# Kernel tuning notes

Measured on AMD Instinct MI355X. Metric: run time of the kernel, lower is better.

The kernel has to match this reference:

```python
import jax, jax.numpy as jnp
import numpy as np

K = 2  # diffusion order
N, S, D, L, C = 4000, 32, 128, 2, 10
THETA = 0.5


def setup_inputs() -> dict:
    key = jax.random.key(0)
    ks = jax.random.split(key, 16)
    w = 0.05  # weight scale to keep tanh/exp in sane range
    return {
        "A": jax.random.uniform(ks[0], (N, N), dtype=jnp.float32),
        "embs": jax.random.normal(ks[1], (L, S, N, D), dtype=jnp.float32),
        "conv1_w": jax.random.normal(ks[2], (K, D, D), dtype=jnp.float32) * w,
        "conv2_w": jax.random.normal(ks[3], (K, D, D), dtype=jnp.float32) * w,
        "lin_in_w": jax.random.normal(ks[4], (D, D), dtype=jnp.float32) * w,
        "lin_out_w": jax.random.normal(ks[5], (D, 2 * D), dtype=jnp.float32) * w,
        "W_psi": jax.random.normal(ks[6], (2 * D, D), dtype=jnp.float32) * w,
        "b_psi": jax.random.normal(ks[7], (D,), dtype=jnp.float32) * w,
        "ae": jax.random.uniform(ks[8], (N, 1, 1), dtype=jnp.float32),
        "ab": jax.random.uniform(ks[9], (N, 1, 1), dtype=jnp.float32),
        "emb_table": jax.random.uniform(ks[10], (N, D), minval=-0.1, maxval=0.1, dtype=jnp.float32),
        "W_p": jax.random.normal(ks[11], (D, C), dtype=jnp.float32) * w,
        "W_c": jax.random.normal(ks[12], (D, D), dtype=jnp.float32) * w,
    }


def _diffusion(A_tilde, X, W):
    # A_tilde: [N,N] (sym-normalized); X: [N,S,D] (linear in X, so batching over S
    # is identical to the per-timestep loop); W: [K,D,D]
    P_f = A_tilde / A_tilde.sum(axis=1, keepdims=True)
    P_v = A_tilde.T / A_tilde.sum(axis=0, keepdims=True)
    Z = jnp.einsum('mn,nsd->msd', P_f, X) @ W[0]
    P_psi_f, P_psi_v = P_f, P_v
    for k in range(1, K):
        if k < K // 2:
            P_psi_f = P_psi_f @ P_f
            M = P_psi_f
        else:
            P_psi_v = P_psi_v @ P_v
            M = P_psi_v
        Z = Z + jnp.einsum('mn,nsd->msd', M, X) @ W[k]
    return Z


def _attention(context, lin_in_w, lin_out_w, ae, ab):
    # context: [N,S,D]; query is the last timestep, output_len == 1
    q = context[:, -1, :] @ lin_in_w.T                    # [N,D]
    scores = jnp.einsum('nd,nsd->ns', q, context)         # [N,S]
    attw = jax.nn.softmax(scores, axis=-1)                # [N,S]
    mix = attw[:, None, :] * context.transpose(0, 2, 1)   # [N,D,S]
    delta_t = jnp.arange(S - 1, -1, -1, dtype=context.dtype)  # flipped arange
    bt = jnp.exp(-ab * delta_t[None, None, :])            # [N,1,S]
    term2 = jax.nn.relu(ae * mix * bt)                    # [N,D,S]
    mix_sum = (term2 + mix).sum(axis=-1)                  # [N,D]
    combined = jnp.concatenate([mix_sum, q], axis=-1)     # [N,2D]
    return jnp.tanh(combined @ lin_out_w.T)               # [N,D]


def reference(A, embs, conv1_w, conv2_w, lin_in_w, lin_out_w, W_psi, b_psi,
              ae, ab, emb_table, W_p, W_c):
    n = A.shape[0]
    A_t = A + jnp.eye(n, dtype=A.dtype)
    d_inv_sqrt = A_t.sum(axis=1) ** -0.5
    A_tilde = d_inv_sqrt[:, None] * A_t * d_inv_sqrt[None, :]

    outs = []
    for l in range(L):
        X = embs[l].transpose(1, 0, 2)                    # [N,S,D]
        h = _diffusion(A_tilde, X, conv1_w)
        h = jax.nn.relu(h)
        h = _diffusion(A_tilde, h, conv2_w)               # [N,S,D]
        # fusion with theta = 0.5 (h_tilde is the raw embedding)
        fused = jnp.concatenate([THETA * h, (1.0 - THETA) * X], axis=-1) @ W_psi + b_psi
        outs.append(_attention(fused, lin_in_w, lin_out_w, ae, ab))
    outputs = jnp.stack(outs)                             # [L,N,D]

    # embedding lookup over arange(N) is an identity gather
    qs = jax.nn.relu(emb_table)                           # [N,D]
    betas = jnp.exp(jnp.einsum('nd,lne->lde', qs, jnp.tanh(outputs)))  # [L,D,D]
    betas = betas / betas.sum(axis=0)
    Z = jnp.einsum('lnd,lde->ne', outputs, betas)         # [N,D]

    P = jax.nn.softmax(Z @ W_p, axis=1)                   # [N,C]
    C_mat = P.T @ Z                                       # [C,D]
    eta = P.T @ A @ P                                     # [C,C] (vectorized eta_ij)
    C_prime = jax.nn.relu(eta @ (C_mat @ W_c.T))          # [C,D]
    return P @ C_prime                                    # [N,D]
```

## Files before the change

### kernel.cpp

```cpp
#include <hip/hip_runtime.h>
#include <hip/hip_bf16.h>


typedef __attribute__((ext_vector_type(8))) short short8;
typedef __attribute__((ext_vector_type(4))) float f32x4;
typedef __attribute__((ext_vector_type(4))) unsigned short us4;

__device__ __forceinline__ unsigned short f2bf(float x) {
  unsigned int u = __builtin_bit_cast(unsigned int, x);
  u += 0x7FFFu + ((u >> 16) & 1u);
  return (unsigned short)(u >> 16);
}

__device__ __forceinline__ void gload16(const void* g, void* l) {
  __builtin_amdgcn_global_load_lds((const __attribute__((address_space(1))) void*)g,
                                   (__attribute__((address_space(3))) void*)l, 16, 0, 0);
}

__device__ __forceinline__ void barrier_() {
  __builtin_amdgcn_sched_barrier(0);
  asm volatile("" ::: "memory");
  __builtin_amdgcn_s_barrier();
  asm volatile("" ::: "memory");
  __builtin_amdgcn_sched_barrier(0);
}
__device__ __forceinline__ void lgkm0() {
  asm volatile("s_waitcnt lgkmcnt(0)" ::: "memory");
  __builtin_amdgcn_sched_barrier(0);
}

template<int TRANS, int RELU>
__global__ __launch_bounds__(512, 2)
void gemm256(const unsigned short* __restrict__ Ap, int lda,
             const unsigned short* __restrict__ Bp, int ldb,
             unsigned short* __restrict__ outp, int ldo, int K)
{
  __shared__ alignas(16) unsigned short lds[81920];
  const int t = threadIdx.x;
  const int lane = t & 63;
  const int wave = t >> 6;
  const int wm = wave >> 2;
  const int wn = wave & 3;
  const int lrow = lane & 15;
  const int kgrp = lane >> 4;
  const int slotbase = (kgrp ^ (lrow & 7)) << 3;

  const int b = blockIdx.x;
  const int wg = (b & 7) * 32 + (b >> 3);
  const int m0 = (wg >> 4) << 8;
  const int j0 = (wg & 15) << 8;

  const int prow = t >> 3;
  const int lslot = (t & 7) ^ (prow & 7);
  const unsigned short* srcA = Ap + (size_t)(m0 + prow) * lda + lslot * 8;
  const unsigned short* srcB = Bp + (size_t)(j0 + prow) * ldb + lslot * 8;
  const size_t a64 = (size_t)64 * lda, a128 = (size_t)128 * lda;
  const size_t b64 = (size_t)64 * ldb, b128 = (size_t)128 * ldb;
  unsigned short* dA = &lds[t * 8];
  unsigned short* dB = &lds[32768 + t * 8];
  const int NT = K >> 6;

#define STG_A(h, kb, kt) { const unsigned short* s_ = srcA + (h)*a128 + (size_t)(kt)*64; \
    gload16(s_, dA + (kb)*16384 + (h)*8192); \
    gload16(s_ + a64, dA + (kb)*16384 + (h)*8192 + 4096); }
#define STG_B(h, bb, kt) { const unsigned short* s_ = srcB + (h)*b128 + (size_t)(kt)*64; \
    gload16(s_, dB + (bb)*16384 + (h)*8192); \
    gload16(s_ + b64, dB + (bb)*16384 + (h)*8192 + 4096); }

  const int arb = wm * 8192 + lrow * 64 + slotbase;
  const int brb = 32768 + (wn >> 1) * 8192 + ((wn & 1) << 12) + lrow * 64 + slotbase;

#define RD_A(dst, base_off) \
  _Pragma("unroll") for (int mf_ = 0; mf_ < 4; ++mf_) { \
    dst[mf_][0] = *(const short8*)&lds[(base_off) + mf_*1024]; \
    dst[mf_][1] = *(const short8*)&lds[((base_off) ^ 32) + mf_*1024]; }
#define RD_B(dst, base_off) \
  _Pragma("unroll") for (int nf_ = 0; nf_ < 2; ++nf_) { \
    dst[nf_][0] = *(const short8*)&lds[(base_off) + nf_*1024]; \
    dst[nf_][1] = *(const short8*)&lds[((base_off) ^ 32) + nf_*1024]; }

#define MFMA16(AF, BF, MB, NB) \
  _Pragma("unroll") for (int mf_ = 0; mf_ < 4; ++mf_) \
  _Pragma("unroll") for (int nf_ = 0; nf_ < 2; ++nf_) { \
    acc[(MB)+mf_][(NB)+nf_] = __builtin_amdgcn_mfma_f32_16x16x32_bf16(AF[mf_][0], BF[nf_][0], acc[(MB)+mf_][(NB)+nf_], 0,0,0); \
    acc[(MB)+mf_][(NB)+nf_] = __builtin_amdgcn_mfma_f32_16x16x32_bf16(AF[mf_][1], BF[nf_][1], acc[(MB)+mf_][(NB)+nf_], 0,0,0); }

  f32x4 acc[8][4];
#pragma unroll
  for (int i = 0; i < 8; ++i)
#pragma unroll
    for (int j = 0; j < 4; ++j) acc[i][j] = f32x4{0.f, 0.f, 0.f, 0.f};

  short8 a0[4][2], a1[4][2], bv[2][2];

  STG_A(0, 0, 0); STG_A(1, 0, 0); STG_B(0, 0, 0); STG_B(1, 0, 0);
  STG_A(0, 1, 1); STG_A(1, 1, 1); STG_B(0, 1, 1); STG_B(1, 1, 1);
  asm volatile("s_waitcnt vmcnt(8)" ::: "memory");
  barrier_();

  int rb3 = 0, sb3 = 2;
  for (int V = 0; V < NT; ++V) {
    const int ab = (V & 1) << 14;
    const int bb = rb3 << 14;
    const bool stg = (V + 2 < NT);
    RD_A(a0, ab + arb);
    RD_B(bv, bb + brb);
    if (stg) STG_B(0, sb3, V + 2);
    barrier_(); lgkm0();
    __builtin_amdgcn_s_setprio(1);
    MFMA16(a0, bv, 0, 0);
    __builtin_amdgcn_s_setprio(0);
    barrier_();
    RD_A(a1, ab + arb + 4096);
    if (stg) STG_B(1, sb3, V + 2);
    barrier_(); lgkm0();
    __builtin_amdgcn_s_setprio(1);
    MFMA16(a1, bv, 4, 0);
    __builtin_amdgcn_s_setprio(0);
    barrier_();
    RD_B(bv, bb + brb + 2048);
    if (stg) STG_A(0, (V & 1), V + 2);
    barrier_(); lgkm0();
    __builtin_amdgcn_s_setprio(1);
    MFMA16(a1, bv, 4, 2);
    __builtin_amdgcn_s_setprio(0);
    barrier_();
    if (stg) STG_A(1, (V & 1), V + 2);
    __builtin_amdgcn_s_setprio(1);
    MFMA16(a0, bv, 0, 2);
    __builtin_amdgcn_s_setprio(0);
    if (stg)             { asm volatile("s_waitcnt vmcnt(8)" ::: "memory"); }
    else if (V + 1 < NT) { asm volatile("s_waitcnt vmcnt(0)" ::: "memory"); }
    barrier_();
    rb3 = (rb3 == 2) ? 0 : rb3 + 1;
    sb3 = (sb3 == 2) ? 0 : sb3 + 1;
  }

#pragma unroll
  for (int mf = 0; mf < 8; ++mf) {
#pragma unroll
    for (int nf = 0; nf < 4; ++nf) {
      const int m = m0 + wm * 128 + mf * 16 + kgrp * 4;
      const int j = j0 + wn * 64 + nf * 16 + lrow;
      if (TRANS) {
        us4 pk;
#pragma unroll
        for (int r = 0; r < 4; ++r) pk[r] = f2bf(acc[mf][nf][r]);
        *(us4*)(outp + (size_t)j * ldo + m) = pk;
      } else {
#pragma unroll
        for (int r = 0; r < 4; ++r) {
          float v = acc[mf][nf][r];
          if (RELU) v = fmaxf(v, 0.f);
          outp[(size_t)(m + r) * ldo + j] = f2bf(v);
        }
      }
    }
  }
#undef STG_A
#undef STG_B
#undef RD_A
#undef RD_B
#undef MFMA16
}

template<int EPI, int RELU, int BIAS>
__global__ __launch_bounds__(256)
void gemm_nt(const unsigned short* __restrict__ A1,
             const unsigned short* __restrict__ A2,
             int k_switch, int a_zstride, int lda,
             const unsigned short* __restrict__ B, int ldb,
             void* __restrict__ outp,
             long o_j, long o_m, long o_z, long o_jt,
             const float* __restrict__ bias, int K)
{
  __shared__ alignas(16) unsigned short At[128*32];
  __shared__ alignas(16) unsigned short Bt[128*32];
  const int t = threadIdx.x;
  const int lane = t & 63;
  const int wave = t >> 6;
  const int m0 = blockIdx.x << 7;
  const int jt = blockIdx.y;
  const int j0 = jt << 7;
  const int z  = blockIdx.z;
  const int wm = (wave >> 1) << 6;
  const int wn = (wave & 1) << 6;
  const int lrow = lane & 15;
  const int kgrp = lane >> 4;

  const unsigned short* A1z = A1 + (long)z * a_zstride;
  const unsigned short* A2z = A2 + (long)z * a_zstride;

  f32x4 acc[4][4];
#pragma unroll
  for (int i = 0; i < 4; ++i)
#pragma unroll
    for (int j = 0; j < 4; ++j) acc[i][j] = f32x4{0.f, 0.f, 0.f, 0.f};

  const int r0 = t >> 2, q0 = t & 3;
  const int c1 = t + 256;
  const int r1 = c1 >> 2, q1 = c1 & 3;

  for (int k0 = 0; k0 < K; k0 += 32) {
    const unsigned short* As; int ka;
    if (k0 < k_switch) { As = A1z; ka = k0; } else { As = A2z; ka = k0 - k_switch; }
    gload16(As + (long)(m0 + r0) * lda + ka + q0 * 8, At + t * 8);
    gload16(As + (long)(m0 + r1) * lda + ka + q1 * 8, At + c1 * 8);
    gload16(B  + (long)(j0 + r0) * ldb + k0 + q0 * 8, Bt + t * 8);
    gload16(B  + (long)(j0 + r1) * ldb + k0 + q1 * 8, Bt + c1 * 8);
    __syncthreads();
    short8 af[4], bv[4];
#pragma unroll
    for (int i = 0; i < 4; ++i)
      af[i] = *(const short8*)(At + (wm + i * 16 + lrow) * 32 + kgrp * 8);
#pragma unroll
    for (int i = 0; i < 4; ++i)
      bv[i] = *(const short8*)(Bt + (wn + i * 16 + lrow) * 32 + kgrp * 8);
#pragma unroll
    for (int i = 0; i < 4; ++i)
#pragma unroll
      for (int j = 0; j < 4; ++j)
        acc[i][j] = __builtin_amdgcn_mfma_f32_16x16x32_bf16(af[i], bv[j], acc[i][j], 0, 0, 0);
    __syncthreads();
  }

  const int mlb = wm + kgrp * 4;
#pragma unroll
  for (int i = 0; i < 4; ++i) {
#pragma unroll
    for (int j = 0; j < 4; ++j) {
      const int jl = wn + j * 16 + lrow;
      const int ml = mlb + i * 16;
      if (EPI == 0) {
        long base = (long)jl * o_j + (long)(m0 + ml) * o_m + (long)z * o_z + (long)jt * o_jt;
        us4 pk;
#pragma unroll
        for (int r = 0; r < 4; ++r) pk[r] = f2bf(acc[i][j][r]);
        *(us4*)((unsigned short*)outp + base) = pk;
      } else {
        float* of = (float*)outp;
        float badd = BIAS ? bias[j0 + jl] : 0.f;
#pragma unroll
        for (int r = 0; r < 4; ++r) {
          long idx = (long)jl * o_j + (long)(m0 + ml + r) * o_m + (long)z * o_z + (long)jt * o_jt;
          of[idx] = acc[i][j][r] + badd;
        }
      }
    }
  }
}

__global__ __launch_bounds__(256) void rowsum_dis(const float* __restrict__ A,
                                                  float* __restrict__ dis) {
  int m = blockIdx.x;
  if (m >= 4000) { if (threadIdx.x == 0) dis[m] = 0.f; return; }
  const float* r = A + (long)m * 4000;
  float a = 0.f;
  for (int i = threadIdx.x; i < 1000; i += 256) {
    float4 v = ((const float4*)r)[i];
    a += v.x + v.y + v.z + v.w;
  }
  for (int o = 32; o; o >>= 1) a += __shfl_xor(a, o);
  __shared__ float ls[4];
  if ((threadIdx.x & 63) == 0) ls[threadIdx.x >> 6] = a;
  __syncthreads();
  if (threadIdx.x == 0) dis[m] = rsqrtf(1.f + ls[0] + ls[1] + ls[2] + ls[3]);
}

__global__ __launch_bounds__(256) void wrow_kernel(const float* __restrict__ A,
                                                   const float* __restrict__ dis,
                                                   float* __restrict__ iwrow) {
  int m = blockIdx.x;
  if (m >= 4000) { if (threadIdx.x == 0) iwrow[m] = 0.f; return; }
  const float* r = A + (long)m * 4000;
  float a = 0.f;
  for (int n = threadIdx.x; n < 4000; n += 256) a += r[n] * dis[n];
  for (int o = 32; o; o >>= 1) a += __shfl_xor(a, o);
  __shared__ float ls[4];
  if ((threadIdx.x & 63) == 0) ls[threadIdx.x >> 6] = a;
  __syncthreads();
  if (threadIdx.x == 0) iwrow[m] = 1.f / (ls[0] + ls[1] + ls[2] + ls[3] + dis[m]);
}

__global__ __launch_bounds__(256) void wcol_part(const float* __restrict__ A,
                                                 const float* __restrict__ dis,
                                                 float* __restrict__ part) {
  int j = blockIdx.x * 256 + threadIdx.x;
  int mz = blockIdx.y;
  float a = 0.f;
  if (j < 4000) {
    int ms = mz * 125;
    for (int m = ms; m < ms + 125; ++m) a += A[(long)m * 4000 + j] * dis[m];
  }
  part[(long)mz * 4096 + j] = a;
}

__global__ __launch_bounds__(256) void wcol_fin(const float* __restrict__ part,
                                                const float* __restrict__ dis,
                                                float* __restrict__ iwcol) {
  int j = blockIdx.x * 256 + threadIdx.x;
  float s = 0.f;
  for (int z = 0; z < 32; ++z) s += part[(long)z * 4096 + j];
  iwcol[j] = (j < 4000) ? 1.f / (s + dis[j]) : 0.f;
}

__global__ __launch_bounds__(256) void build_P(const float* __restrict__ A,
                                               const float* __restrict__ dis,
                                               const float* __restrict__ iwrow,
                                               const float* __restrict__ iwcol,
                                               unsigned short* __restrict__ Pcat,
                                               unsigned short* __restrict__ PV,
                                               unsigned short* __restrict__ PVT) {
  __shared__ float tile[64][65];
  int m0 = blockIdx.y * 64, n0 = blockIdx.x * 64;
#pragma unroll
  for (int i = 0; i < 16; ++i) {
    int idx = i * 256 + threadIdx.x;
    int lr = idx >> 6, lc = idx & 63;
    int m = m0 + lr, n = n0 + lc;
    float v = 0.f;
    if (m < 4000 && n < 4000) {
      float a = A[(long)m * 4000 + n];
      if (m == n) a += 1.f;
      v = a * dis[n];
    }
    Pcat[(long)m * 8192 + n] = f2bf(v * iwrow[m]);
    float pv = v * iwcol[m];
    PVT[(long)m * 4096 + n] = f2bf(pv);
    tile[lr][lc] = pv;
  }
  __syncthreads();
#pragma unroll
  for (int i = 0; i < 16; ++i) {
    int idx = i * 256 + threadIdx.x;
    int lr = idx >> 6, lc = idx & 63;
    PV[(long)(n0 + lr) * 4096 + (m0 + lc)] = f2bf(tile[lc][lr]);
  }
}

__global__ __launch_bounds__(256) void prep_weights(const float* __restrict__ lin_in,
                                                    const float* __restrict__ lin_out,
                                                    const float* __restrict__ c1,
                                                    const float* __restrict__ c2,
                                                    const float* __restrict__ wpsi,
                                                    float* __restrict__ LWiT, float* __restrict__ LWoT,
                                                    unsigned short* __restrict__ CW1T,
                                                    unsigned short* __restrict__ CW2T,
                                                    unsigned short* __restrict__ WPST) {
  int i = blockIdx.x * 256 + threadIdx.x;
  if (i < 16384) {
    int e = i >> 7, d = i & 127;
    LWiT[e * 128 + d] = lin_in[d * 128 + e];
  } else if (i < 49152) {
    int k = i - 16384; int ii = k >> 7, d = k & 127;
    LWoT[k] = lin_out[d * 256 + ii];
  } else if (i < 81920) {
    int k = i - 49152; int j = k >> 7, kk = k & 127;
    CW1T[k] = f2bf(c1[(j >> 7) * 16384 + kk * 128 + (j & 127)]);
  } else if (i < 114688) {
    int k = i - 81920; int j = k >> 7, kk = k & 127;
    CW2T[k] = f2bf(c2[(j >> 7) * 16384 + kk * 128 + (j & 127)]);
  } else if (i < 147456) {
    int k = i - 114688; int e = k >> 8, d2 = k & 255;
    WPST[k] = f2bf(0.5f * wpsi[d2 * 128 + e]);
  }
}

__global__ __launch_bounds__(256) void convert_X(const float* __restrict__ embsL,
                                                 unsigned short* __restrict__ X) {
  long i4 = (long)blockIdx.x * 256 + threadIdx.x;
  long e = i4 << 2;
  int n = (int)(e >> 12);
  int r = (int)(e & 4095);
  us4 o;
  if (n < 4000) {
    int s = r >> 7, d = r & 127;
    float4 v = *(const float4*)(embsL + ((long)s * 4000 + n) * 128 + d);
    o[0] = f2bf(v.x); o[1] = f2bf(v.y); o[2] = f2bf(v.z); o[3] = f2bf(v.w);
  } else { o[0] = o[1] = o[2] = o[3] = 0; }
  *(us4*)(X + (long)n * 4096 + r) = o;
}

__global__ __launch_bounds__(128) void attention_kernel(const float* __restrict__ F,
                                                        const float* __restrict__ LWiT,
                                                        const float* __restrict__ LWoT,
                                                        const float* __restrict__ ae,
                                                        const float* __restrict__ ab,
                                                        float* __restrict__ outp) {
  int n = blockIdx.x, t = threadIdx.x;
  __shared__ float Fs[32 * 132];
  __shared__ float qv[128], msum[128], attw[32], btv[32];
  const float* Fr = F + (long)n * 4096;
  for (int i = t; i < 4096; i += 128) { int s = i >> 7, d = i & 127; Fs[s * 132 + d] = Fr[i]; }
  __syncthreads();
  {
    float a = 0.f;
    const float* Frow = Fs + 31 * 132;
    for (int e = 0; e < 128; ++e) a += Frow[e] * LWiT[e * 128 + t];
    qv[t] = a;
  }
  __syncthreads();
  if (t < 32) {
    float sc = 0.f;
    for (int d = 0; d < 128; ++d) sc += qv[d] * Fs[t * 132 + d];
    float mx = sc;
    for (int o = 16; o; o >>= 1) mx = fmaxf(mx, __shfl_xor(mx, o, 32));
    float ex = expf(sc - mx), sm = ex;
    for (int o = 16; o; o >>= 1) sm += __shfl_xor(sm, o, 32);
    attw[t] = ex / sm;
  } else if (t >= 64 && t < 96) {
    int s = t - 64;
    btv[s] = expf(-ab[n] * (float)(31 - s));
  }
  __syncthreads();
  {
    float aen = ae[n], acc = 0.f;
    for (int s = 0; s < 32; ++s) {
      float f = Fs[s * 132 + t];
      acc += attw[s] * (f + aen * btv[s] * fmaxf(f, 0.f));
    }
    msum[t] = acc;
  }
  __syncthreads();
  {
    float a = 0.f;
    for (int e = 0; e < 128; ++e) a += msum[e] * LWoT[e * 128 + t];
    for (int e = 0; e < 128; ++e) a += qv[e] * LWoT[(e + 128) * 128 + t];
    outp[(long)n * 128 + t] = tanhf(a);
  }
}

__global__ __launch_bounds__(256) void tanh_qs(const float* __restrict__ outs,
                                               const float* __restrict__ embt,
                                               float* __restrict__ T, float* __restrict__ qs) {
  long i = (long)blockIdx.x * 256 + threadIdx.x;
  if (i < 1024000) T[i] = tanhf(outs[i]);
  else { long j = i - 1024000; if (j < 512000) qs[j] = fmaxf(embt[j], 0.f); }
}

__global__ __launch_bounds__(256) void betas_raw_kernel(const float* __restrict__ qs,
                                                        const float* __restrict__ T,
                                                        float* __restrict__ braw) {
  int e = threadIdx.x & 127, dl = threadIdx.x >> 7;
  int d = blockIdx.x * 2 + dl, l = blockIdx.y;
  const float* Tl = T + (long)l * 512000;
  float acc = 0.f;
  for (int n = 0; n < 4000; ++n) acc += qs[(long)n * 128 + d] * Tl[(long)n * 128 + e];
  braw[((long)l * 128 + d) * 128 + e] = acc;
}

__global__ __launch_bounds__(256) void bnorm_kernel(const float* __restrict__ braw,
                                                    float* __restrict__ bn) {
  int i = blockIdx.x * 256 + threadIdx.x;
  float b0 = expf(braw[i]), b1 = expf(braw[16384 + i]);
  float s = b0 + b1;
  bn[i] = b0 / s;
  bn[16384 + i] = b1 / s;
}

__global__ __launch_bounds__(256) void z_kernel(const float* __restrict__ outs,
                                                const float* __restrict__ bn,
                                                float* __restrict__ Zb) {
  int n = blockIdx.x * 2 + (threadIdx.x >> 7);
  int e = threadIdx.x & 127;
  float acc = 0.f;
  for (int l = 0; l < 2; ++l) {
    const float* orow = outs + ((long)l * 4000 + n) * 128;
    const float* brow = bn + (long)l * 16384;
    for (int d = 0; d < 128; ++d) acc += orow[d] * brow[d * 128 + e];
  }
  Zb[(long)n * 128 + e] = acc;
}

__global__ __launch_bounds__(256) void p_kernel(const float* __restrict__ Zb,
                                                const float* __restrict__ Wp,
                                                float* __restrict__ P) {
  int n = blockIdx.x * 4 + (threadIdx.x >> 6);
  int c = threadIdx.x & 63;
  float val = 0.f;
  if (c < 10) {
    const float* zr = Zb + (long)n * 128;
    for (int d = 0; d < 128; ++d) val += zr[d] * Wp[d * 10 + c];
  }
  float mx = val;
  for (int i = 0; i < 10; ++i) mx = fmaxf(mx, __shfl(val, i, 64));
  float ex = (c < 10) ? expf(val - mx) : 0.f;
  float sm = 0.f;
  for (int i = 0; i < 10; ++i) sm += __shfl(ex, i, 64);
  if (c < 12) P[(long)n * 12 + c] = (c < 10) ? ex / sm : 0.f;
}

__global__ __launch_bounds__(256) void ap_kernel(const float* __restrict__ A,
                                                 const float* __restrict__ P,
                                                 float* __restrict__ AP) {
  int m = blockIdx.x, t = threadIdx.x;
  const float* Ar = A + (long)m * 4000;
  float acc[10];
#pragma unroll
  for (int c = 0; c < 10; ++c) acc[c] = 0.f;
  for (int n = t; n < 4000; n += 256) {
    float a = Ar[n];
    const float* Pr = P + (long)n * 12;
#pragma unroll
    for (int c = 0; c < 10; ++c) acc[c] += a * Pr[c];
  }
#pragma unroll
  for (int c = 0; c < 10; ++c)
    for (int o = 32; o; o >>= 1) acc[c] += __shfl_xor(acc[c], o);
  __shared__ float ls[4][10];
  if ((t & 63) == 0)
    for (int c = 0; c < 10; ++c) ls[t >> 6][c] = acc[c];
  __syncthreads();
  if (t < 10) AP[(long)m * 12 + t] = ls[0][t] + ls[1][t] + ls[2][t] + ls[3][t];
  if (t >= 10 && t < 12) AP[(long)m * 12 + t] = 0.f;
}

__global__ __launch_bounds__(256) void etacm_part(const float* __restrict__ P,
                                                  const float* __restrict__ AP,
                                                  const float* __restrict__ Z,
                                                  float* __restrict__ peta,
                                                  float* __restrict__ pcm) {
  int b = blockIdx.x, t = threadIdx.x;
  int ms = b * 63, me = ms + 63; if (me > 4000) me = 4000;
  int i_ = t / 10, j_ = t % 10;
  float ea = 0.f;
  float ca[5];
#pragma unroll
  for (int k = 0; k < 5; ++k) ca[k] = 0.f;
  for (int m = ms; m < me; ++m) {
    if (t < 100) ea += P[(long)m * 12 + i_] * AP[(long)m * 12 + j_];
#pragma unroll
    for (int k = 0; k < 5; ++k) {
      int idx = t + 256 * k;
      int c = idx >> 7, e = idx & 127;
      ca[k] += P[(long)m * 12 + c] * Z[(long)m * 128 + e];
    }
  }
  if (t < 100) peta[(long)b * 100 + t] = ea;
#pragma unroll
  for (int k = 0; k < 5; ++k) pcm[(long)b * 1280 + t + 256 * k] = ca[k];
}

__global__ __launch_bounds__(256) void final_small(const float* __restrict__ peta,
                                                   const float* __restrict__ pcm,
                                                   const float* __restrict__ Wc,
                                                   float* __restrict__ cprime) {
  __shared__ float eta_s[100], cm_s[1280], tmp_s[1280];
  int t = threadIdx.x;
  if (t < 100) {
    float s = 0.f;
    for (int b = 0; b < 64; ++b) s += peta[(long)b * 100 + t];
    eta_s[t] = s;
  }
  for (int i = t; i < 1280; i += 256) {
    float s = 0.f;
    for (int b = 0; b < 64; ++b) s += pcm[(long)b * 1280 + i];
    cm_s[i] = s;
  }
  __syncthreads();
  for (int i = t; i < 1280; i += 256) {
    int c = i >> 7, d = i & 127;
    float s = 0.f;
    for (int e = 0; e < 128; ++e) s += cm_s[c * 128 + e] * Wc[d * 128 + e];
    tmp_s[i] = s;
  }
  __syncthreads();
  for (int i = t; i < 1280; i += 256) {
    int c = i >> 7, d = i & 127;
    float s = 0.f;
    for (int j = 0; j < 10; ++j) s += eta_s[c * 10 + j] * tmp_s[j * 128 + d];
    cprime[i] = fmaxf(s, 0.f);
  }
}

__global__ __launch_bounds__(256) void out_kernel(const float* __restrict__ P,
                                                  const float* __restrict__ cpr,
                                                  float* __restrict__ out) {
  int idx = blockIdx.x * 256 + threadIdx.x;
  int n = idx >> 7, d = idx & 127;
  float s = 0.f;
#pragma unroll
  for (int c = 0; c < 10; ++c) s += P[(long)n * 12 + c] * cpr[c * 128 + d];
  out[idx] = s;
}

extern "C" void kernel_launch(void* const* d_in, const int* in_sizes, int n_in,
                              void* d_out, int out_size, void* d_ws, size_t ws_size,
                              hipStream_t stream) {
  (void)in_sizes; (void)n_in; (void)out_size; (void)ws_size;
  const float* A      = (const float*)d_in[0];
  const float* embs   = (const float*)d_in[1];
  const float* conv1w = (const float*)d_in[2];
  const float* conv2w = (const float*)d_in[3];
  const float* lin_in = (const float*)d_in[4];
  const float* lin_out= (const float*)d_in[5];
  const float* Wpsi   = (const float*)d_in[6];
  const float* bpsi   = (const float*)d_in[7];
  const float* ae     = (const float*)d_in[8];
  const float* ab     = (const float*)d_in[9];
  const float* embt   = (const float*)d_in[10];
  const float* Wp     = (const float*)d_in[11];
  const float* Wc     = (const float*)d_in[12];
  float* out = (float*)d_out;
  char* ws = (char*)d_ws;

  size_t off = 0;
  auto alloc = [&](size_t b) { size_t r = off; off += (b + 255) & ~(size_t)255; return r; };
  unsigned short* PCAT = (unsigned short*)(ws + alloc((size_t)4096 * 8192 * 2));
  char*           BTF  = ws + alloc((size_t)4096 * 8192 * 2);
  unsigned short* BT   = (unsigned short*)BTF;
  float*          Ff   = (float*)BTF;
  unsigned short* XBF  = (unsigned short*)(ws + alloc((size_t)4096 * 4096 * 2));
  unsigned short* PV   = XBF;
  unsigned short* HBUF = (unsigned short*)(ws + alloc((size_t)4096 * 4096 * 2));
  unsigned short* PVT  = HBUF;
  float* DIS   = (float*)(ws + alloc(4096 * 4));
  float* IWROW = (float*)(ws + alloc(4096 * 4));
  float* IWCOL = (float*)(ws + alloc(4096 * 4));
  float* WCP   = (float*)(ws + alloc((size_t)32 * 4096 * 4));
  float* LWIT  = (float*)(ws + alloc(16384 * 4));
  float* LWOT  = (float*)(ws + alloc(32768 * 4));
  unsigned short* CW1T = (unsigned short*)(ws + alloc(32768 * 2));
  unsigned short* CW2T = (unsigned short*)(ws + alloc(32768 * 2));
  unsigned short* WPST = (unsigned short*)(ws + alloc(32768 * 2));
  float* OUTS = (float*)(ws + alloc((size_t)2 * 4000 * 128 * 4));
  float* TT   = (float*)(ws + alloc((size_t)2 * 4000 * 128 * 4));
  float* QS   = (float*)(ws + alloc((size_t)4000 * 128 * 4));
  float* BRAW = (float*)(ws + alloc(32768 * 4));
  float* BNRM = (float*)(ws + alloc(32768 * 4));
  float* ZB   = (float*)(ws + alloc((size_t)4000 * 128 * 4));
  float* PP   = (float*)(ws + alloc((size_t)4000 * 12 * 4));
  float* APB  = (float*)(ws + alloc((size_t)4000 * 12 * 4));
  float* PETA = (float*)(ws + alloc((size_t)64 * 100 * 4));
  float* PCM  = (float*)(ws + alloc((size_t)64 * 1280 * 4));
  float* CPR  = (float*)(ws + alloc(1280 * 4));

  const int BIG = 1 << 30;

  rowsum_dis<<<4096, 256, 0, stream>>>(A, DIS);
  wrow_kernel<<<4096, 256, 0, stream>>>(A, DIS, IWROW);
  wcol_part<<<dim3(16, 32), 256, 0, stream>>>(A, DIS, WCP);
  wcol_fin<<<16, 256, 0, stream>>>(WCP, DIS, IWCOL);
  prep_weights<<<576, 256, 0, stream>>>(lin_in, lin_out, conv1w, conv2w, Wpsi,
                                        LWIT, LWOT, CW1T, CW2T, WPST);
  build_P<<<dim3(64, 64), 256, 0, stream>>>(A, DIS, IWROW, IWCOL, PCAT, PV, PVT);

  gemm256<1, 0><<<256, 512, 0, stream>>>(PVT, 4096, PV, 4096, PCAT + 4096, 8192, 4096);

  for (int l = 0; l < 2; ++l) {
    convert_X<<<16384, 256, 0, stream>>>(embs + (long)l * 32 * 4000 * 128, XBF);
    gemm_nt<0, 0, 0><<<dim3(32, 2, 32), 256, 0, stream>>>(
        XBF, XBF, BIG, 128, 4096, CW1T, 128,
        BT, 8192L, 1L, 128L * 8192, 4096L, nullptr, 128);
    gemm256<0, 1><<<256, 512, 0, stream>>>(PCAT, 8192, BT, 8192, HBUF, 4096, 8192);
    gemm_nt<0, 0, 0><<<dim3(32, 2, 32), 256, 0, stream>>>(
        HBUF, HBUF, BIG, 128, 4096, CW2T, 128,
        BT, 8192L, 1L, 128L * 8192, 4096L, nullptr, 128);
    gemm256<0, 0><<<256, 512, 0, stream>>>(PCAT, 8192, BT, 8192, HBUF, 4096, 8192);
    gemm_nt<2, 0, 1><<<dim3(32, 1, 32), 256, 0, stream>>>(
        HBUF, XBF, 128, 128, 4096, WPST, 256,
        Ff, 1L, 4096L, 128L, 0L, bpsi, 256);
    attention_kernel<<<4000, 128, 0, stream>>>(Ff, LWIT, LWOT, ae, ab,
                                               OUTS + (long)l * 512000);
  }

  tanh_qs<<<6000, 256, 0, stream>>>(OUTS, embt, TT, QS);
  betas_raw_kernel<<<dim3(64, 2), 256, 0, stream>>>(QS, TT, BRAW);
  bnorm_kernel<<<64, 256, 0, stream>>>(BRAW, BNRM);
  z_kernel<<<2000, 256, 0, stream>>>(OUTS, BNRM, ZB);
  p_kernel<<<1000, 256, 0, stream>>>(ZB, Wp, PP);
  ap_kernel<<<4000, 256, 0, stream>>>(A, PP, APB);
  etacm_part<<<64, 256, 0, stream>>>(PP, APB, ZB, PETA, PCM);
  final_small<<<1, 256, 0, stream>>>(PETA, PCM, Wc, CPR);
  out_kernel<<<2000, 256, 0, stream>>>(PP, CPR, out);
}
```

Baseline: 1.583 ms.

## Software-pipeline LDS fragment reads across MFMA phases in gemm256 main loop

Restructures the main loop of the 256-tile GEMM so LDS fragment reads for the next phase (and the next K-tile's A and B fragments) are issued before the current MFMA block. It uses partial lgkmcnt waits instead of full waits and drops roughly half the barriers per iteration. The aim is to hide LDS read latency behind matrix-core work and cut synchronisation stalls. The cost is extra fragment registers (b1) under a 2-blocks-per-CU launch bound, and more delicate buffer-reuse ordering with vmcnt tuning.

```diff
diff --git a/kernel.cpp b/kernel.cpp
--- a/kernel.cpp
+++ b/kernel.cpp
@@ -22,10 +22,6 @@
   asm volatile("" ::: "memory");
   __builtin_amdgcn_s_barrier();
   asm volatile("" ::: "memory");
-  __builtin_amdgcn_sched_barrier(0);
-}
-__device__ __forceinline__ void lgkm0() {
-  asm volatile("s_waitcnt lgkmcnt(0)" ::: "memory");
   __builtin_amdgcn_sched_barrier(0);
 }
 
@@ -68,7 +64,7 @@
     gload16(s_ + b64, dB + (bb)*16384 + (h)*8192 + 4096); }
 
   const int arb = wm * 8192 + lrow * 64 + slotbase;
-  const int brb = 32768 + (wn >> 1) * 8192 + ((wn & 1) << 12) + lrow * 64 + slotbase;
+  const int brb = (wn >> 1) * 8192 + ((wn & 1) << 12) + lrow * 64 + slotbase;
 
 #define RD_A(dst, base_off) \
   _Pragma("unroll") for (int mf_ = 0; mf_ < 4; ++mf_) { \
@@ -85,54 +81,68 @@
     acc[(MB)+mf_][(NB)+nf_] = __builtin_amdgcn_mfma_f32_16x16x32_bf16(AF[mf_][0], BF[nf_][0], acc[(MB)+mf_][(NB)+nf_], 0,0,0); \
     acc[(MB)+mf_][(NB)+nf_] = __builtin_amdgcn_mfma_f32_16x16x32_bf16(AF[mf_][1], BF[nf_][1], acc[(MB)+mf_][(NB)+nf_], 0,0,0); }
 
+#define LGKM(n) { asm volatile("s_waitcnt lgkmcnt(" #n ")" ::: "memory"); \
+                  __builtin_amdgcn_sched_barrier(0); }
+
   f32x4 acc[8][4];
 #pragma unroll
   for (int i = 0; i < 8; ++i)
 #pragma unroll
     for (int j = 0; j < 4; ++j) acc[i][j] = f32x4{0.f, 0.f, 0.f, 0.f};
 
-  short8 a0[4][2], a1[4][2], bv[2][2];
-
-  STG_A(0, 0, 0); STG_A(1, 0, 0); STG_B(0, 0, 0); STG_B(1, 0, 0);
-  STG_A(0, 1, 1); STG_A(1, 1, 1); STG_B(0, 1, 1); STG_B(1, 1, 1);
+  short8 a0[4][2], a1[4][2], b0[2][2], b1[2][2];
+
+  STG_B(0, 0, 0); STG_B(1, 0, 0); STG_A(0, 0, 0); STG_A(1, 0, 0);
+  STG_B(0, 1, 1); STG_B(1, 1, 1); STG_A(0, 1, 1); STG_A(1, 1, 1);
   asm volatile("s_waitcnt vmcnt(8)" ::: "memory");
   barrier_();
-
-  int rb3 = 0, sb3 = 2;
+  RD_A(a0, arb);
+  RD_B(b0, 32768 + brb);
+
+  int rb3 = 0, rn3 = 1, sb3 = 2;
   for (int V = 0; V < NT; ++V) {
-    const int ab = (V & 1) << 14;
-    const int bb = rb3 << 14;
+    const int abuf  = (V & 1) << 14;
+    const int anbuf = ((V + 1) & 1) << 14;
+    const int bbuf  = 32768 + (rb3 << 14);
+    const int bnbuf = 32768 + (rn3 << 14);
     const bool stg = (V + 2 < NT);
-    RD_A(a0, ab + arb);
-    RD_B(bv, bb + brb);
+    const bool rdn = (V + 1 < NT);
+
+    RD_B(b1, bbuf + brb + 2048);
+    LGKM(4);
     if (stg) STG_B(0, sb3, V + 2);
-    barrier_(); lgkm0();
     __builtin_amdgcn_s_setprio(1);
-    MFMA16(a0, bv, 0, 0);
+    MFMA16(a0, b0, 0, 0);
     __builtin_amdgcn_s_setprio(0);
     barrier_();
-    RD_A(a1, ab + arb + 4096);
+
+    RD_A(a1, abuf + arb + 4096);
+    LGKM(8);
     if (stg) STG_B(1, sb3, V + 2);
-    barrier_(); lgkm0();
     __builtin_amdgcn_s_setprio(1);
-    MFMA16(a1, bv, 4, 0);
+    MFMA16(a0, b1, 0, 2);
+    __builtin_amdgcn_s_setprio(0);
+    if (stg) { asm volatile("s_waitcnt vmcnt(4)" ::: "memory"); }
+    else     { asm volatile("s_waitcnt vmcnt(0)" ::: "memory"); }
+    barrier_();
+
+    if (rdn) { RD_A(a0, anbuf + arb); LGKM(8); }
+    else     { LGKM(0); }
+    if (stg) STG_A(0, (V & 1), V + 2);
+    __builtin_amdgcn_s_setprio(1);
+    MFMA16(a1, b0, 4, 0);
     __builtin_amdgcn_s_setprio(0);
     barrier_();
-    RD_B(bv, bb + brb + 2048);
-    if (stg) STG_A(0, (V & 1), V + 2);
-    barrier_(); lgkm0();
+
+    if (rdn) { RD_B(b0, bnbuf + brb); LGKM(4); }
+    else     { LGKM(0); }
+    if (stg) STG_A(1, (V & 1), V + 2);
     __builtin_amdgcn_s_setprio(1);
-    MFMA16(a1, bv, 4, 2);
+    MFMA16(a1, b1, 4, 2);
     __builtin_amdgcn_s_setprio(0);
     barrier_();
-    if (stg) STG_A(1, (V & 1), V + 2);
-    __builtin_amdgcn_s_setprio(1);
-    MFMA16(a0, bv, 0, 2);
-    __builtin_amdgcn_s_setprio(0);
-    if (stg)             { asm volatile("s_waitcnt vmcnt(8)" ::: "memory"); }
-    else if (V + 1 < NT) { asm volatile("s_waitcnt vmcnt(0)" ::: "memory"); }
-    barrier_();
-    rb3 = (rb3 == 2) ? 0 : rb3 + 1;
+
+    rb3 = rn3; rn3 = (rn3 == 2) ? 0 : rn3 + 1;
     sb3 = (sb3 == 2) ? 0 : sb3 + 1;
   }
 
@@ -162,6 +172,7 @@
 #undef RD_A
 #undef RD_B
 #undef MFMA16
+#undef LGKM
 }
 
 template<int EPI, int RELU, int BIAS>
```

Result: faster. 1.544 ms (median of 3 runs) (-2.4%).
